# Performance work log

Measured on AMD Instinct MI355X. Metric: run time of the kernel, lower is better.

The kernel has to match this reference:

```python
import jax, jax.numpy as jnp
import numpy as np

DIM = 8192
BATCH = 8

def setup_inputs() -> dict:
    key = jax.random.key(0)
    k1, k2 = jax.random.split(key)
    sdr = jax.random.normal(k1, (BATCH, DIM), dtype=jnp.float32)
    # scale synapse so sigmoid inputs stay in a reasonable range (weights clamped to [-1,1] in torch)
    synapse = jax.random.normal(k2, (DIM, DIM), dtype=jnp.float32) * (1.0 / np.sqrt(DIM))
    return {"sdr": sdr, "synapse": synapse, "steps": 2, "top_k": 60}

def reference(sdr, synapse, steps, top_k):
    # activation propagation: GEMV/GEMM -> sigmoid -> top-k sparsification per step
    act = sdr.astype(jnp.float32)
    B, N = act.shape
    rows = jnp.arange(B)[:, None]  # [B,1] row indices for scatter
    k = min(int(top_k), N)
    for _ in range(int(steps)):
        act = jax.nn.sigmoid(act @ synapse.T)          # [B,N]
        vals, idx = jax.lax.top_k(act, k)              # [B,k]
        act = jnp.zeros_like(act).at[rows, idx].set(vals)  # keep only top-k activations
    return act
```

## Files before the change

kernel.cpp:

```cpp
#include <hip/hip_runtime.h>
#include <cstdint>


#define DIM 8192
#define BATCH 8

__device__ __forceinline__ float sigmoidf_(float x) {
    return 1.0f / (1.0f + __expf(-x));
}

__global__ __launch_bounds__(256) void gemv8_sigmoid(
    const float* __restrict__ A,
    const float* __restrict__ W,
    float* __restrict__ Y)
{
    const int lane = threadIdx.x & 63;
    const int wid  = threadIdx.x >> 6;
    const int row0 = blockIdx.x * 4;
    const int jbeg = wid * (DIM / 4);
    const int jend = jbeg + (DIM / 4);
    const int jl   = lane * 4;

    float acc[4][8];
#pragma unroll
    for (int r = 0; r < 4; ++r)
#pragma unroll
        for (int b = 0; b < 8; ++b) acc[r][b] = 0.0f;

    for (int j0 = jbeg; j0 < jend; j0 += 256) {
        float4 a[8];
#pragma unroll
        for (int b = 0; b < 8; ++b)
            a[b] = *(const float4*)(A + b * DIM + j0 + jl);
        float4 wv[4];
#pragma unroll
        for (int r = 0; r < 4; ++r)
            wv[r] = *(const float4*)(W + (size_t)(row0 + r) * DIM + j0 + jl);
#pragma unroll
        for (int r = 0; r < 4; ++r) {
#pragma unroll
            for (int b = 0; b < 8; ++b) {
                acc[r][b] += wv[r].x * a[b].x;
                acc[r][b] += wv[r].y * a[b].y;
                acc[r][b] += wv[r].z * a[b].z;
                acc[r][b] += wv[r].w * a[b].w;
            }
        }
    }

    __shared__ float part[4][4][8];
#pragma unroll
    for (int r = 0; r < 4; ++r) {
#pragma unroll
        for (int b = 0; b < 8; ++b) {
            float v = acc[r][b];
#pragma unroll
            for (int off = 32; off > 0; off >>= 1)
                v += __shfl_down(v, off, 64);
            if (lane == 0) part[wid][r][b] = v;
        }
    }
    __syncthreads();

    if (threadIdx.x < 32) {
        const int r = threadIdx.x >> 3;
        const int b = threadIdx.x & 7;
        const float s = part[0][r][b] + part[1][r][b]
                      + part[2][r][b] + part[3][r][b];
        Y[b * DIM + row0 + r] = sigmoidf_(s);
    }
}

__global__ __launch_bounds__(256) void topk_sparsify(
    const float* __restrict__ Yin,
    float* __restrict__ Yout,
    const int* __restrict__ kptr)
{
    const int row  = blockIdx.x;
    const int tid  = threadIdx.x;
    const int lane = tid & 63;
    const int wid  = tid >> 6;
    int k = kptr ? *kptr : 60;
    if (k > DIM) k = DIM;

    uint32_t v[32];
    const float* src = Yin + (size_t)row * DIM;
#pragma unroll
    for (int i = 0; i < 32; ++i)
        v[i] = __float_as_uint(src[tid + i * 256]);

    __shared__ int s_part[4];
    __shared__ int s_ctr;

    uint32_t lo = 0u, hi = 0x3F800000u;
    while (hi - lo > 1u) {
        const uint32_t mid = lo + ((hi - lo) >> 1);
        int c = 0;
#pragma unroll
        for (int i = 0; i < 32; ++i) c += (v[i] >= mid) ? 1 : 0;
#pragma unroll
        for (int off = 32; off > 0; off >>= 1)
            c += __shfl_down(c, off, 64);
        if (lane == 0) s_part[wid] = c;
        __syncthreads();
        const int tot = s_part[0] + s_part[1] + s_part[2] + s_part[3];
        __syncthreads();
        if (tot >= k) lo = mid; else hi = mid;
    }
    const uint32_t cutoff = lo;

    int needg = 0;
    {
        int c = 0;
#pragma unroll
        for (int i = 0; i < 32; ++i) c += (v[i] > cutoff) ? 1 : 0;
#pragma unroll
        for (int off = 32; off > 0; off >>= 1)
            c += __shfl_down(c, off, 64);
        if (lane == 0) s_part[wid] = c;
        if (tid == 0) s_ctr = 0;
        __syncthreads();
        needg = s_part[0] + s_part[1] + s_part[2] + s_part[3];
    }
    const int need_eq = k - needg;

    float* dst = Yout + (size_t)row * DIM;
#pragma unroll
    for (int i = 0; i < 32; ++i) {
        const uint32_t b = v[i];
        float val = 0.0f;
        if (b > cutoff) {
            val = __uint_as_float(b);
        } else if (b == cutoff) {
            const int pos = atomicAdd(&s_ctr, 1);
            if (pos < need_eq) val = __uint_as_float(b);
        }
        dst[tid + i * 256] = val;
    }
}

extern "C" void kernel_launch(void* const* d_in, const int* in_sizes, int n_in,
                              void* d_out, int out_size, void* d_ws, size_t ws_size,
                              hipStream_t stream) {
    const float* sdr = (const float*)d_in[0];
    const float* syn = (const float*)d_in[1];
    const int* kptr  = (n_in > 3) ? (const int*)d_in[3] : nullptr;
    float* out = (float*)d_out;
    float* tmp = (float*)d_ws;

    gemv8_sigmoid<<<2048, 256, 0, stream>>>(sdr, syn, out);
    topk_sparsify<<<8, 256, 0, stream>>>(out, out, kptr);
    gemv8_sigmoid<<<2048, 256, 0, stream>>>(out, syn, tmp);
    topk_sparsify<<<8, 256, 0, stream>>>(tmp, out, kptr);
}
```

Measured before the change: 458.7 us.

## Split GEMV over K into partial sums, stage activations in LDS, fuse reduction into top-k

```diff
diff --git a/kernel.cpp b/kernel.cpp
--- a/kernel.cpp
+++ b/kernel.cpp
@@ -4,42 +4,55 @@
 
 #define DIM 8192
 #define BATCH 8
+#define KPARTS 8
+#define KRANGE (DIM / KPARTS)
+#define ROWS_PB 32
+#define WIN 256
 
-__device__ __forceinline__ float sigmoidf_(float x) {
-    return 1.0f / (1.0f + __expf(-x));
-}
-
-__global__ __launch_bounds__(256) void gemv8_sigmoid(
+__global__ __launch_bounds__(256) void gemv_part(
     const float* __restrict__ A,
     const float* __restrict__ W,
-    float* __restrict__ Y)
+    float* __restrict__ P)
 {
-    const int lane = threadIdx.x & 63;
-    const int wid  = threadIdx.x >> 6;
-    const int row0 = blockIdx.x * 4;
-    const int jbeg = wid * (DIM / 4);
-    const int jend = jbeg + (DIM / 4);
-    const int jl   = lane * 4;
+    __shared__ float As[BATCH][KRANGE];
 
-    float acc[4][8];
+    const int tid  = threadIdx.x;
+    const int lane = tid & 63;
+    const int wid  = tid >> 6;
+    const int p     = blockIdx.x & (KPARTS - 1);
+    const int chunk = blockIdx.x >> 3;
+    const int jbeg  = p * KRANGE;
+
+    {
+        const int j = tid * 4;
 #pragma unroll
-    for (int r = 0; r < 4; ++r)
+        for (int b = 0; b < BATCH; ++b)
+            *(float4*)(&As[b][j]) = *(const float4*)(A + b * DIM + jbeg + j);
+    }
+    __syncthreads();
+
+    const int wrow0 = chunk * ROWS_PB + wid * 8;
+
+    float acc[8][BATCH];
 #pragma unroll
-        for (int b = 0; b < 8; ++b) acc[r][b] = 0.0f;
+    for (int r = 0; r < 8; ++r)
+#pragma unroll
+        for (int b = 0; b < BATCH; ++b) acc[r][b] = 0.0f;
 
-    for (int j0 = jbeg; j0 < jend; j0 += 256) {
+    for (int w = 0; w < KRANGE; w += WIN) {
+        const int j = w + lane * 4;
+        float4 wv[8];
+#pragma unroll
+        for (int r = 0; r < 8; ++r)
+            wv[r] = *(const float4*)(W + (size_t)(wrow0 + r) * DIM + jbeg + j);
         float4 a[8];
 #pragma unroll
-        for (int b = 0; b < 8; ++b)
-            a[b] = *(const float4*)(A + b * DIM + j0 + jl);
-        float4 wv[4];
+        for (int b = 0; b < BATCH; ++b)
+            a[b] = *(const float4*)(&As[b][j]);
 #pragma unroll
-        for (int r = 0; r < 4; ++r)
-            wv[r] = *(const float4*)(W + (size_t)(row0 + r) * DIM + j0 + jl);
+        for (int r = 0; r < 8; ++r) {
 #pragma unroll
-        for (int r = 0; r < 4; ++r) {
-#pragma unroll
-            for (int b = 0; b < 8; ++b) {
+            for (int b = 0; b < BATCH; ++b) {
                 acc[r][b] += wv[r].x * a[b].x;
                 acc[r][b] += wv[r].y * a[b].y;
                 acc[r][b] += wv[r].z * a[b].z;
@@ -48,31 +61,22 @@
         }
     }
 
-    __shared__ float part[4][4][8];
 #pragma unroll
-    for (int r = 0; r < 4; ++r) {
+    for (int r = 0; r < 8; ++r) {
 #pragma unroll
-        for (int b = 0; b < 8; ++b) {
+        for (int b = 0; b < BATCH; ++b) {
             float v = acc[r][b];
 #pragma unroll
             for (int off = 32; off > 0; off >>= 1)
                 v += __shfl_down(v, off, 64);
-            if (lane == 0) part[wid][r][b] = v;
+            if (lane == 0)
+                P[(size_t)(b * KPARTS + p) * DIM + wrow0 + r] = v;
         }
-    }
-    __syncthreads();
-
-    if (threadIdx.x < 32) {
-        const int r = threadIdx.x >> 3;
-        const int b = threadIdx.x & 7;
-        const float s = part[0][r][b] + part[1][r][b]
-                      + part[2][r][b] + part[3][r][b];
-        Y[b * DIM + row0 + r] = sigmoidf_(s);
     }
 }
 
-__global__ __launch_bounds__(256) void topk_sparsify(
-    const float* __restrict__ Yin,
+__global__ __launch_bounds__(256) void topk_combine(
+    const float* __restrict__ P,
     float* __restrict__ Yout,
     const int* __restrict__ kptr)
 {
@@ -84,13 +88,20 @@
     if (k > DIM) k = DIM;
 
     uint32_t v[32];
-    const float* src = Yin + (size_t)row * DIM;
+    const float* src = P + (size_t)row * KPARTS * DIM;
 #pragma unroll
-    for (int i = 0; i < 32; ++i)
-        v[i] = __float_as_uint(src[tid + i * 256]);
+    for (int i = 0; i < 32; ++i) {
+        const int idx = tid + i * 256;
+        float x = 0.0f;
+#pragma unroll
+        for (int pp = 0; pp < KPARTS; ++pp)
+            x += src[pp * DIM + idx];
+        v[i] = __float_as_uint(1.0f / (1.0f + __expf(-x)));
+    }
 
-    __shared__ int s_part[4];
+    __shared__ int s_part[2][4];
     __shared__ int s_ctr;
+    int pb = 0;
 
     uint32_t lo = 0u, hi = 0x3F800000u;
     while (hi - lo > 1u) {
@@ -101,15 +112,16 @@
 #pragma unroll
         for (int off = 32; off > 0; off >>= 1)
             c += __shfl_down(c, off, 64);
-        if (lane == 0) s_part[wid] = c;
+        if (lane == 0) s_part[pb][wid] = c;
         __syncthreads();
-        const int tot = s_part[0] + s_part[1] + s_part[2] + s_part[3];
-        __syncthreads();
+        const int tot = s_part[pb][0] + s_part[pb][1]
+                      + s_part[pb][2] + s_part[pb][3];
+        pb ^= 1;
         if (tot >= k) lo = mid; else hi = mid;
     }
     const uint32_t cutoff = lo;
 
-    int needg = 0;
+    int needg;
     {
         int c = 0;
 #pragma unroll
@@ -117,10 +129,11 @@
 #pragma unroll
         for (int off = 32; off > 0; off >>= 1)
             c += __shfl_down(c, off, 64);
-        if (lane == 0) s_part[wid] = c;
+        if (lane == 0) s_part[pb][wid] = c;
         if (tid == 0) s_ctr = 0;
         __syncthreads();
-        needg = s_part[0] + s_part[1] + s_part[2] + s_part[3];
+        needg = s_part[pb][0] + s_part[pb][1]
+              + s_part[pb][2] + s_part[pb][3];
     }
     const int need_eq = k - needg;
 
@@ -146,10 +159,10 @@
     const float* syn = (const float*)d_in[1];
     const int* kptr  = (n_in > 3) ? (const int*)d_in[3] : nullptr;
     float* out = (float*)d_out;
-    float* tmp = (float*)d_ws;
+    float* P   = (float*)d_ws;
 
-    gemv8_sigmoid<<<2048, 256, 0, stream>>>(sdr, syn, out);
-    topk_sparsify<<<8, 256, 0, stream>>>(out, out, kptr);
-    gemv8_sigmoid<<<2048, 256, 0, stream>>>(out, syn, tmp);
-    topk_sparsify<<<8, 256, 0, stream>>>(tmp, out, kptr);
+    gemv_part<<<(DIM / ROWS_PB) * KPARTS, 256, 0, stream>>>(sdr, syn, P);
+    topk_combine<<<BATCH, 256, 0, stream>>>(P, out, kptr);
+    gemv_part<<<(DIM / ROWS_PB) * KPARTS, 256, 0, stream>>>(out, syn, P);
+    topk_combine<<<BATCH, 256, 0, stream>>>(P, out, kptr);
 }
```

Measured after the change: 629.0 us. +37.1%, slower.

## Restructure GEMV to two rows per wave with split-K halves, double-buffer top-k counts

Applied to the files above, without the earlier changes.

```diff
diff --git a/kernel.cpp b/kernel.cpp
--- a/kernel.cpp
+++ b/kernel.cpp
@@ -9,65 +9,62 @@
     return 1.0f / (1.0f + __expf(-x));
 }
 
-__global__ __launch_bounds__(256) void gemv8_sigmoid(
+__global__ __launch_bounds__(256, 8) void gemv8_sigmoid(
     const float* __restrict__ A,
     const float* __restrict__ W,
     float* __restrict__ Y)
 {
     const int lane = threadIdx.x & 63;
     const int wid  = threadIdx.x >> 6;
-    const int row0 = blockIdx.x * 4;
-    const int jbeg = wid * (DIM / 4);
-    const int jend = jbeg + (DIM / 4);
-    const int jl   = lane * 4;
+    const int rp   = blockIdx.x * 2 + (wid >> 1);
+    const int kh   = wid & 1;
+    const int i0   = rp * 2;
+    const int jbeg = kh * (DIM / 2);
 
-    float acc[4][8];
+    float acc0[BATCH], acc1[BATCH];
 #pragma unroll
-    for (int r = 0; r < 4; ++r)
+    for (int b = 0; b < BATCH; ++b) { acc0[b] = 0.0f; acc1[b] = 0.0f; }
+
+    const float* wp0 = W + (size_t)i0 * DIM + jbeg + lane * 4;
+    const float* wp1 = wp0 + DIM;
+    const float* ap  = A + jbeg + lane * 4;
+
+#pragma unroll 1
+    for (int w = 0; w < DIM / 2; w += 256) {
+        const float4 w0 = *(const float4*)wp0;
+        const float4 w1 = *(const float4*)wp1;
 #pragma unroll
-        for (int b = 0; b < 8; ++b) acc[r][b] = 0.0f;
-
-    for (int j0 = jbeg; j0 < jend; j0 += 256) {
-        float4 a[8];
-#pragma unroll
-        for (int b = 0; b < 8; ++b)
-            a[b] = *(const float4*)(A + b * DIM + j0 + jl);
-        float4 wv[4];
-#pragma unroll
-        for (int r = 0; r < 4; ++r)
-            wv[r] = *(const float4*)(W + (size_t)(row0 + r) * DIM + j0 + jl);
-#pragma unroll
-        for (int r = 0; r < 4; ++r) {
-#pragma unroll
-            for (int b = 0; b < 8; ++b) {
-                acc[r][b] += wv[r].x * a[b].x;
-                acc[r][b] += wv[r].y * a[b].y;
-                acc[r][b] += wv[r].z * a[b].z;
-                acc[r][b] += wv[r].w * a[b].w;
-            }
+        for (int b = 0; b < BATCH; ++b) {
+            const float4 a = *(const float4*)(ap + b * DIM);
+            acc0[b] += w0.x * a.x + w0.y * a.y + w0.z * a.z + w0.w * a.w;
+            acc1[b] += w1.x * a.x + w1.y * a.y + w1.z * a.z + w1.w * a.w;
         }
+        wp0 += 256; wp1 += 256; ap += 256;
     }
 
-    __shared__ float part[4][4][8];
+    __shared__ float part[2][2][2][BATCH];
 #pragma unroll
-    for (int r = 0; r < 4; ++r) {
+    for (int b = 0; b < BATCH; ++b) {
+        float v0 = acc0[b], v1 = acc1[b];
 #pragma unroll
-        for (int b = 0; b < 8; ++b) {
-            float v = acc[r][b];
-#pragma unroll
-            for (int off = 32; off > 0; off >>= 1)
-                v += __shfl_down(v, off, 64);
-            if (lane == 0) part[wid][r][b] = v;
+        for (int off = 32; off > 0; off >>= 1) {
+            v0 += __shfl_down(v0, off, 64);
+            v1 += __shfl_down(v1, off, 64);
+        }
+        if (lane == 0) {
+            part[wid >> 1][kh][0][b] = v0;
+            part[wid >> 1][kh][1][b] = v1;
         }
     }
     __syncthreads();
 
     if (threadIdx.x < 32) {
-        const int r = threadIdx.x >> 3;
-        const int b = threadIdx.x & 7;
-        const float s = part[0][r][b] + part[1][r][b]
-                      + part[2][r][b] + part[3][r][b];
-        Y[b * DIM + row0 + r] = sigmoidf_(s);
+        const int b  = threadIdx.x & 7;
+        const int r  = (threadIdx.x >> 3) & 1;
+        const int q  = threadIdx.x >> 4;
+        const float s = part[q][0][r][b] + part[q][1][r][b];
+        const int row = (blockIdx.x * 2 + q) * 2 + r;
+        Y[b * DIM + row] = sigmoidf_(s);
     }
 }
 
@@ -89,8 +86,9 @@
     for (int i = 0; i < 32; ++i)
         v[i] = __float_as_uint(src[tid + i * 256]);
 
-    __shared__ int s_part[4];
+    __shared__ int s_part[2][4];
     __shared__ int s_ctr;
+    int pb = 0;
 
     uint32_t lo = 0u, hi = 0x3F800000u;
     while (hi - lo > 1u) {
@@ -101,15 +99,16 @@
 #pragma unroll
         for (int off = 32; off > 0; off >>= 1)
             c += __shfl_down(c, off, 64);
-        if (lane == 0) s_part[wid] = c;
+        if (lane == 0) s_part[pb][wid] = c;
         __syncthreads();
-        const int tot = s_part[0] + s_part[1] + s_part[2] + s_part[3];
-        __syncthreads();
+        const int tot = s_part[pb][0] + s_part[pb][1]
+                      + s_part[pb][2] + s_part[pb][3];
+        pb ^= 1;
         if (tot >= k) lo = mid; else hi = mid;
     }
     const uint32_t cutoff = lo;
 
-    int needg = 0;
+    int needg;
     {
         int c = 0;
 #pragma unroll
@@ -117,10 +116,11 @@
 #pragma unroll
         for (int off = 32; off > 0; off >>= 1)
             c += __shfl_down(c, off, 64);
-        if (lane == 0) s_part[wid] = c;
+        if (lane == 0) s_part[pb][wid] = c;
         if (tid == 0) s_ctr = 0;
         __syncthreads();
-        needg = s_part[0] + s_part[1] + s_part[2] + s_part[3];
+        needg = s_part[pb][0] + s_part[pb][1]
+              + s_part[pb][2] + s_part[pb][3];
     }
     const int need_eq = k - needg;
 
```

After: 485.1 us. 5.8% more time.
